# Performance work log

Hardware: AMD Instinct MI355X
Metric: run time of the kernel (lower is better)

## Reference

```python
import jax, jax.numpy as jnp
import numpy as np

T, B = 100, 256
NUM_IN, NUM_HID, NUM_OUT = 784, 512, 10
BETA = 0.95
THRESH = 1.0   # snntorch Leaky default threshold
SLOPE = 25.0   # surrogate.fast_sigmoid default slope

# Heaviside spike with fast_sigmoid surrogate gradient (snntorch semantics)
@jax.custom_vjp
def spike_fn(x):
    return (x > 0).astype(x.dtype)

def _spike_fwd(x):
    return spike_fn(x), x

def _spike_bwd(x, g):
    return (g / (SLOPE * jnp.abs(x) + 1.0) ** 2,)

spike_fn.defvjp(_spike_fwd, _spike_bwd)

def setup_inputs() -> dict:
    key = jax.random.key(0)
    ks = jax.random.split(key, 5)
    x = jax.random.normal(ks[0], (T, B, NUM_IN), dtype=jnp.float32)
    w1 = jax.random.normal(ks[1], (NUM_HID, NUM_IN), dtype=jnp.float32) / np.float32(np.sqrt(NUM_IN))
    b1 = jax.random.normal(ks[2], (NUM_HID,), dtype=jnp.float32) * 0.01
    w2 = jax.random.normal(ks[3], (NUM_OUT, NUM_HID), dtype=jnp.float32) / np.float32(np.sqrt(NUM_HID))
    b2 = jax.random.normal(ks[4], (NUM_OUT,), dtype=jnp.float32) * 0.01
    return {"x": x, "w1": w1, "b1": b1, "w2": w2, "b2": b2}

def _snn_forward(x, w1, b1, w2, b2):
    mem1_0 = jnp.zeros((B, NUM_HID), x.dtype)
    mem2_0 = jnp.zeros((B, NUM_OUT), x.dtype)

    def step(carry, xt):
        mem1, mem2 = carry
        # layer 1: Linear + Leaky (reset-by-subtraction, reset detached as in snntorch)
        cur1 = xt @ w1.T + b1
        reset1 = jax.lax.stop_gradient(spike_fn(mem1 - THRESH))
        mem1 = BETA * mem1 + cur1 - reset1 * THRESH
        spk1 = spike_fn(mem1 - THRESH)
        # layer 2
        cur2 = spk1 @ w2.T + b2
        reset2 = jax.lax.stop_gradient(spike_fn(mem2 - THRESH))
        mem2 = BETA * mem2 + cur2 - reset2 * THRESH
        spk2 = spike_fn(mem2 - THRESH)
        return (mem1, mem2), (cur2, spk2, spk1, mem2, mem1)

    _, ys = jax.lax.scan(step, (mem1_0, mem2_0), x)
    # ys = (cur_list, spk_list, spk_hidden_list, mem_list, mem_hidden_list), stacked over T
    return ys

def reference(x, w1, b1, w2, b2):
    return _snn_forward(x, w1, b1, w2, b2)
```

## Files before the change

kernel.cpp:

```cpp
#include <hip/hip_runtime.h>
#include <stdint.h>

#define T_STEPS 100
#define BATCH   256
#define NIN     784
#define NHID    512
#define NOUT    10


#define BM 128
#define BN 128
#define BK 8
#define PANEL_K 384

__global__ __launch_bounds__(256) void gemm1_dual(
    const float* __restrict__ X, const float* __restrict__ W,
    float* __restrict__ C1, float* __restrict__ C2)
{
    __shared__ float As[2][BK][BM + 4];
    __shared__ float Bs[2][BK][BN + 4];

    const int tid = threadIdx.x;
    const int bm  = blockIdx.x * BM;
    const int bn  = blockIdx.y * BN;
    const int kb  = blockIdx.z ? PANEL_K : 0;
    float* __restrict__ C = blockIdx.z ? C2 : C1;

    const int row  = tid >> 1;
    const int koff = (tid & 1) * 4;

    const int w    = tid >> 6;
    const int lane = tid & 63;
    const int tm   = (w & 1) * 64 + (lane & 7) * 8;
    const int tn   = (w >> 1) * 64 + (lane >> 3) * 8;

    float acc[8][8];
    #pragma unroll
    for (int i = 0; i < 8; ++i)
        #pragma unroll
        for (int j = 0; j < 8; ++j) acc[i][j] = 0.f;

    const float* Xp = X + (size_t)(bm + row) * NIN + kb + koff;
    const float* Wp = W + (size_t)(bn + row) * NIN + kb + koff;

    float4 pa = *(const float4*)(Xp);
    float4 pb = *(const float4*)(Wp);
    As[0][koff+0][row] = pa.x; As[0][koff+1][row] = pa.y;
    As[0][koff+2][row] = pa.z; As[0][koff+3][row] = pa.w;
    Bs[0][koff+0][row] = pb.x; Bs[0][koff+1][row] = pb.y;
    Bs[0][koff+2][row] = pb.z; Bs[0][koff+3][row] = pb.w;

    const int NITER = PANEL_K / BK;
    for (int it = 0; it < NITER; ++it) {
        const int cur = it & 1;
        __syncthreads();

        if (it + 1 < NITER) {
            const int k0 = (it + 1) * BK;
            pa = *(const float4*)(Xp + k0);
            pb = *(const float4*)(Wp + k0);
        }

        #pragma unroll
        for (int kk = 0; kk < BK; ++kk) {
            float4 av0 = *(const float4*)&As[cur][kk][tm];
            float4 av1 = *(const float4*)&As[cur][kk][tm + 4];
            float4 bv0 = *(const float4*)&Bs[cur][kk][tn];
            float4 bv1 = *(const float4*)&Bs[cur][kk][tn + 4];
            float a[8] = {av0.x, av0.y, av0.z, av0.w, av1.x, av1.y, av1.z, av1.w};
            float b[8] = {bv0.x, bv0.y, bv0.z, bv0.w, bv1.x, bv1.y, bv1.z, bv1.w};
            #pragma unroll
            for (int i = 0; i < 8; ++i)
                #pragma unroll
                for (int j = 0; j < 8; ++j)
                    acc[i][j] = fmaf(a[i], b[j], acc[i][j]);
        }

        if (it + 1 < NITER) {
            const int nxt = cur ^ 1;
            As[nxt][koff+0][row] = pa.x; As[nxt][koff+1][row] = pa.y;
            As[nxt][koff+2][row] = pa.z; As[nxt][koff+3][row] = pa.w;
            Bs[nxt][koff+0][row] = pb.x; Bs[nxt][koff+1][row] = pb.y;
            Bs[nxt][koff+2][row] = pb.z; Bs[nxt][koff+3][row] = pb.w;
        }
    }

    #pragma unroll
    for (int i = 0; i < 8; ++i) {
        size_t r = (size_t)(bm + tm + i) * NHID + bn + tn;
        *(float4*)&C[r]     = make_float4(acc[i][0], acc[i][1], acc[i][2], acc[i][3]);
        *(float4*)&C[r + 4] = make_float4(acc[i][4], acc[i][5], acc[i][6], acc[i][7]);
    }
}

__global__ __launch_bounds__(256) void leaky_hidden_fused(
    float* __restrict__ mem_io,
    const float* __restrict__ c2,
    float* __restrict__ spk_out,
    const float* __restrict__ X,
    const float* __restrict__ W1,
    const float* __restrict__ b1)
{
    __shared__ float4 xs4[T_STEPS][4];

    const int tid = threadIdx.x;
    const int idx = blockIdx.x * 256 + tid;
    const size_t STRIDE = (size_t)BATCH * NHID;
    const int h  = idx & (NHID - 1);
    const int bb = idx >> 9;

    {
        const float* xbase = X + (size_t)bb * NIN + 768;
        for (int e = tid; e < T_STEPS * 4; e += 256) {
            const int t = e >> 2, q = e & 3;
            xs4[t][q] = *(const float4*)(xbase + (size_t)t * BATCH * NIN + q * 4);
        }
    }

    const float* wp = W1 + (size_t)h * NIN + 768;
    float4 w0 = *(const float4*)(wp);
    float4 w1v = *(const float4*)(wp + 4);
    float4 w2v = *(const float4*)(wp + 8);
    float4 w3v = *(const float4*)(wp + 12);
    const float wt[16] = {w0.x, w0.y, w0.z, w0.w, w1v.x, w1v.y, w1v.z, w1v.w,
                          w2v.x, w2v.y, w2v.z, w2v.w, w3v.x, w3v.y, w3v.z, w3v.w};
    const float bias = b1[h];

    float buf1[16], buf2[16];
    #pragma unroll
    for (int i = 0; i < 16; ++i) {
        buf1[i] = mem_io[idx + (size_t)i * STRIDE];
        buf2[i] = c2[idx + (size_t)i * STRIDE];
    }

    __syncthreads();

    float a3cur;
    {
        float4 v0 = xs4[0][0], v1 = xs4[0][1], v2 = xs4[0][2], v3 = xs4[0][3];
        float a = 0.f;
        a = fmaf(v0.x, wt[0], a);  a = fmaf(v0.y, wt[1], a);
        a = fmaf(v0.z, wt[2], a);  a = fmaf(v0.w, wt[3], a);
        a = fmaf(v1.x, wt[4], a);  a = fmaf(v1.y, wt[5], a);
        a = fmaf(v1.z, wt[6], a);  a = fmaf(v1.w, wt[7], a);
        a = fmaf(v2.x, wt[8], a);  a = fmaf(v2.y, wt[9], a);
        a = fmaf(v2.z, wt[10], a); a = fmaf(v2.w, wt[11], a);
        a = fmaf(v3.x, wt[12], a); a = fmaf(v3.y, wt[13], a);
        a = fmaf(v3.z, wt[14], a); a = fmaf(v3.w, wt[15], a);
        a3cur = a;
    }

    float mem = 0.f;

    #define LH_BODY(T_, J_)                                                   \
    {                                                                         \
        const int t_ = (T_);                                                  \
        const float p1 = buf1[(J_)];                                          \
        const float p2 = buf2[(J_)];                                          \
        if (t_ + 16 < T_STEPS) {                                              \
            buf1[(J_)] = mem_io[idx + (size_t)(t_ + 16) * STRIDE];            \
            buf2[(J_)] = c2[idx + (size_t)(t_ + 16) * STRIDE];                \
        }                                                                     \
        float a3next = 0.f;                                                   \
        if (t_ + 1 < T_STEPS) {                                               \
            float4 v0 = xs4[t_ + 1][0], v1 = xs4[t_ + 1][1];                  \
            float4 v2 = xs4[t_ + 1][2], v3 = xs4[t_ + 1][3];                  \
            float a = 0.f;                                                    \
            a = fmaf(v0.x, wt[0], a);  a = fmaf(v0.y, wt[1], a);              \
            a = fmaf(v0.z, wt[2], a);  a = fmaf(v0.w, wt[3], a);              \
            a = fmaf(v1.x, wt[4], a);  a = fmaf(v1.y, wt[5], a);              \
            a = fmaf(v1.z, wt[6], a);  a = fmaf(v1.w, wt[7], a);              \
            a = fmaf(v2.x, wt[8], a);  a = fmaf(v2.y, wt[9], a);              \
            a = fmaf(v2.z, wt[10], a); a = fmaf(v2.w, wt[11], a);             \
            a = fmaf(v3.x, wt[12], a); a = fmaf(v3.y, wt[13], a);             \
            a3next = a;                                                       \
            a3next = fmaf(v3.z, wt[14], a3next);                              \
            a3next = fmaf(v3.w, wt[15], a3next);                              \
        }                                                                     \
        const float cur = __fadd_rn(__fadd_rn(__fadd_rn(p1, p2), a3cur), bias); \
        const float rst = (mem > 1.0f) ? 1.0f : 0.0f;                         \
        mem = __fsub_rn(__fadd_rn(__fmul_rn(0.95f, mem), cur), rst);          \
        const size_t off = idx + (size_t)t_ * STRIDE;                         \
        spk_out[off] = (mem > 1.0f) ? 1.0f : 0.0f;                            \
        mem_io[off]  = mem;                                                   \
        a3cur = a3next;                                                       \
    }

    for (int tb = 0; tb < 96; tb += 16) {
        LH_BODY(tb + 0, 0)  LH_BODY(tb + 1, 1)  LH_BODY(tb + 2, 2)  LH_BODY(tb + 3, 3)
        LH_BODY(tb + 4, 4)  LH_BODY(tb + 5, 5)  LH_BODY(tb + 6, 6)  LH_BODY(tb + 7, 7)
        LH_BODY(tb + 8, 8)  LH_BODY(tb + 9, 9)  LH_BODY(tb + 10, 10) LH_BODY(tb + 11, 11)
        LH_BODY(tb + 12, 12) LH_BODY(tb + 13, 13) LH_BODY(tb + 14, 14) LH_BODY(tb + 15, 15)
    }
    LH_BODY(96, 0) LH_BODY(97, 1) LH_BODY(98, 2) LH_BODY(99, 3)

    #undef LH_BODY
}

#define G2_ROWS 32

__global__ __launch_bounds__(320) void gemm2_f64(
    const float* __restrict__ spk1, const float* __restrict__ W2,
    const float* __restrict__ b2, float* __restrict__ cur2)
{
    __shared__ float w2s[NOUT * NHID];
    const int tid = threadIdx.x;
    for (int i = tid; i < NOUT * NHID; i += 320) w2s[i] = W2[i];
    __syncthreads();

    const int r = tid / NOUT;
    const int o = tid % NOUT;
    const size_t m = (size_t)blockIdx.x * G2_ROWS + r;
    const float* rowp = spk1 + m * NHID;
    const float* wp   = w2s + o * NHID;
    double dot = 0.0;
    #pragma unroll 4
    for (int k = 0; k < NHID; k += 4) {
        float4 s  = *(const float4*)(rowp + k);
        float4 wv = *(const float4*)(wp + k);
        dot = fma((double)s.x, (double)wv.x, dot);
        dot = fma((double)s.y, (double)wv.y, dot);
        dot = fma((double)s.z, (double)wv.z, dot);
        dot = fma((double)s.w, (double)wv.w, dot);
    }
    cur2[m * NOUT + o] = (float)(dot + (double)b2[o]);
}

__global__ __launch_bounds__(256) void leaky_out_kernel(
    const float* __restrict__ cur2, float* __restrict__ spk2,
    float* __restrict__ mem2)
{
    const int idx = blockIdx.x * blockDim.x + threadIdx.x;
    if (idx >= BATCH * NOUT) return;
    const int STRIDE = BATCH * NOUT;

    float cur[T_STEPS];
    #pragma unroll
    for (int t = 0; t < T_STEPS; ++t)
        cur[t] = cur2[(size_t)t * STRIDE + idx];

    float mem = 0.f;
    #pragma unroll
    for (int t = 0; t < T_STEPS; ++t) {
        const float rst = (mem > 1.0f) ? 1.0f : 0.0f;
        mem = __fsub_rn(__fadd_rn(__fmul_rn(0.95f, mem), cur[t]), rst);
        const size_t off = (size_t)t * STRIDE + idx;
        spk2[off] = (mem > 1.0f) ? 1.0f : 0.0f;
        mem2[off] = mem;
    }
}

extern "C" void kernel_launch(void* const* d_in, const int* in_sizes, int n_in,
                              void* d_out, int out_size, void* d_ws, size_t ws_size,
                              hipStream_t stream) {
    const float* x  = (const float*)d_in[0];
    const float* w1 = (const float*)d_in[1];
    const float* b1 = (const float*)d_in[2];
    const float* w2 = (const float*)d_in[3];
    const float* b2 = (const float*)d_in[4];

    float* out = (float*)d_out;
    float* cur2_out = out;
    float* spk2_out = out + 256000;
    float* spk1_out = out + 512000;
    float* mem2_out = out + 13619200;
    float* mem1_out = out + 13875200;

    const int M = T_STEPS * BATCH;

    const size_t p2_bytes = (size_t)M * NHID * sizeof(float);
    float* p2buf = (d_ws != nullptr && ws_size >= p2_bytes)
                       ? (float*)d_ws : spk1_out;

    dim3 gp(M / BM, NHID / BN, 2);
    gemm1_dual<<<gp, 256, 0, stream>>>(x, w1, mem1_out, p2buf);

    leaky_hidden_fused<<<(BATCH * NHID) / 256, 256, 0, stream>>>(
        mem1_out, p2buf, spk1_out, x, w1, b1);

    gemm2_f64<<<M / G2_ROWS, 320, 0, stream>>>(spk1_out, w2, b2, cur2_out);

    leaky_out_kernel<<<(BATCH * NOUT + 255) / 256, 256, 0, stream>>>(
        cur2_out, spk2_out, mem2_out);
}
```

Baseline: 482.9 us.

## Split hidden leaky kernel into producer and consumer warps with LDS double buffering

```diff
diff --git a/kernel.cpp b/kernel.cpp
--- a/kernel.cpp
+++ b/kernel.cpp
@@ -93,108 +93,122 @@
     }
 }
 
-__global__ __launch_bounds__(256) void leaky_hidden_fused(
+__global__ __launch_bounds__(512) void leaky_hidden_fused(
     float* __restrict__ mem_io,
-    const float* __restrict__ c2,
-    float* __restrict__ spk_out,
+    const float* c2,
+    float* spk_out,
     const float* __restrict__ X,
     const float* __restrict__ W1,
     const float* __restrict__ b1)
 {
     __shared__ float4 xs4[T_STEPS][4];
-
-    const int tid = threadIdx.x;
-    const int idx = blockIdx.x * 256 + tid;
+    __shared__ float  p1s[2][8][256];
+    __shared__ float  p2s[2][8][256];
+
+    const int tid  = threadIdx.x;
+    const int lane256 = tid & 255;
+    const int base = blockIdx.x * 256;
     const size_t STRIDE = (size_t)BATCH * NHID;
-    const int h  = idx & (NHID - 1);
-    const int bb = idx >> 9;
+    const int bb = base >> 9;
+    const size_t col = (size_t)base + lane256;
 
     {
         const float* xbase = X + (size_t)bb * NIN + 768;
-        for (int e = tid; e < T_STEPS * 4; e += 256) {
+        for (int e = tid; e < T_STEPS * 4; e += 512) {
             const int t = e >> 2, q = e & 3;
             xs4[t][q] = *(const float4*)(xbase + (size_t)t * BATCH * NIN + q * 4);
         }
     }
 
-    const float* wp = W1 + (size_t)h * NIN + 768;
-    float4 w0 = *(const float4*)(wp);
-    float4 w1v = *(const float4*)(wp + 4);
-    float4 w2v = *(const float4*)(wp + 8);
-    float4 w3v = *(const float4*)(wp + 12);
-    const float wt[16] = {w0.x, w0.y, w0.z, w0.w, w1v.x, w1v.y, w1v.z, w1v.w,
-                          w2v.x, w2v.y, w2v.z, w2v.w, w3v.x, w3v.y, w3v.z, w3v.w};
-    const float bias = b1[h];
-
-    float buf1[16], buf2[16];
-    #pragma unroll
-    for (int i = 0; i < 16; ++i) {
-        buf1[i] = mem_io[idx + (size_t)i * STRIDE];
-        buf2[i] = c2[idx + (size_t)i * STRIDE];
+    const bool producer = (tid >= 256);
+
+    float wt[16];
+    float bias = 0.f;
+    float mem  = 0.f;
+
+    if (producer) {
+        float v1[8], v2[8];
+        #pragma unroll
+        for (int j = 0; j < 8; ++j) {
+            v1[j] = mem_io[col + (size_t)j * STRIDE];
+            v2[j] = c2[col + (size_t)j * STRIDE];
+        }
+        #pragma unroll
+        for (int j = 0; j < 8; ++j) {
+            p1s[0][j][lane256] = v1[j];
+            p2s[0][j][lane256] = v2[j];
+        }
+    } else {
+        const int h = (int)(col & (NHID - 1));
+        const float* wp = W1 + (size_t)h * NIN + 768;
+        float4 w0  = *(const float4*)(wp);
+        float4 w1v = *(const float4*)(wp + 4);
+        float4 w2v = *(const float4*)(wp + 8);
+        float4 w3v = *(const float4*)(wp + 12);
+        wt[0]=w0.x;  wt[1]=w0.y;  wt[2]=w0.z;  wt[3]=w0.w;
+        wt[4]=w1v.x; wt[5]=w1v.y; wt[6]=w1v.z; wt[7]=w1v.w;
+        wt[8]=w2v.x; wt[9]=w2v.y; wt[10]=w2v.z; wt[11]=w2v.w;
+        wt[12]=w3v.x; wt[13]=w3v.y; wt[14]=w3v.z; wt[15]=w3v.w;
+        bias = b1[h];
     }
 
     __syncthreads();
 
-    float a3cur;
-    {
-        float4 v0 = xs4[0][0], v1 = xs4[0][1], v2 = xs4[0][2], v3 = xs4[0][3];
-        float a = 0.f;
-        a = fmaf(v0.x, wt[0], a);  a = fmaf(v0.y, wt[1], a);
-        a = fmaf(v0.z, wt[2], a);  a = fmaf(v0.w, wt[3], a);
-        a = fmaf(v1.x, wt[4], a);  a = fmaf(v1.y, wt[5], a);
-        a = fmaf(v1.z, wt[6], a);  a = fmaf(v1.w, wt[7], a);
-        a = fmaf(v2.x, wt[8], a);  a = fmaf(v2.y, wt[9], a);
-        a = fmaf(v2.z, wt[10], a); a = fmaf(v2.w, wt[11], a);
-        a = fmaf(v3.x, wt[12], a); a = fmaf(v3.y, wt[13], a);
-        a = fmaf(v3.z, wt[14], a); a = fmaf(v3.w, wt[15], a);
-        a3cur = a;
-    }
-
-    float mem = 0.f;
-
-    #define LH_BODY(T_, J_)                                                   \
-    {                                                                         \
-        const int t_ = (T_);                                                  \
-        const float p1 = buf1[(J_)];                                          \
-        const float p2 = buf2[(J_)];                                          \
-        if (t_ + 16 < T_STEPS) {                                              \
-            buf1[(J_)] = mem_io[idx + (size_t)(t_ + 16) * STRIDE];            \
-            buf2[(J_)] = c2[idx + (size_t)(t_ + 16) * STRIDE];                \
-        }                                                                     \
-        float a3next = 0.f;                                                   \
-        if (t_ + 1 < T_STEPS) {                                               \
-            float4 v0 = xs4[t_ + 1][0], v1 = xs4[t_ + 1][1];                  \
-            float4 v2 = xs4[t_ + 1][2], v3 = xs4[t_ + 1][3];                  \
-            float a = 0.f;                                                    \
-            a = fmaf(v0.x, wt[0], a);  a = fmaf(v0.y, wt[1], a);              \
-            a = fmaf(v0.z, wt[2], a);  a = fmaf(v0.w, wt[3], a);              \
-            a = fmaf(v1.x, wt[4], a);  a = fmaf(v1.y, wt[5], a);              \
-            a = fmaf(v1.z, wt[6], a);  a = fmaf(v1.w, wt[7], a);              \
-            a = fmaf(v2.x, wt[8], a);  a = fmaf(v2.y, wt[9], a);              \
-            a = fmaf(v2.z, wt[10], a); a = fmaf(v2.w, wt[11], a);             \
-            a = fmaf(v3.x, wt[12], a); a = fmaf(v3.y, wt[13], a);             \
-            a3next = a;                                                       \
-            a3next = fmaf(v3.z, wt[14], a3next);                              \
-            a3next = fmaf(v3.w, wt[15], a3next);                              \
-        }                                                                     \
-        const float cur = __fadd_rn(__fadd_rn(__fadd_rn(p1, p2), a3cur), bias); \
-        const float rst = (mem > 1.0f) ? 1.0f : 0.0f;                         \
-        mem = __fsub_rn(__fadd_rn(__fmul_rn(0.95f, mem), cur), rst);          \
-        const size_t off = idx + (size_t)t_ * STRIDE;                         \
-        spk_out[off] = (mem > 1.0f) ? 1.0f : 0.0f;                            \
-        mem_io[off]  = mem;                                                   \
-        a3cur = a3next;                                                       \
-    }
-
-    for (int tb = 0; tb < 96; tb += 16) {
-        LH_BODY(tb + 0, 0)  LH_BODY(tb + 1, 1)  LH_BODY(tb + 2, 2)  LH_BODY(tb + 3, 3)
-        LH_BODY(tb + 4, 4)  LH_BODY(tb + 5, 5)  LH_BODY(tb + 6, 6)  LH_BODY(tb + 7, 7)
-        LH_BODY(tb + 8, 8)  LH_BODY(tb + 9, 9)  LH_BODY(tb + 10, 10) LH_BODY(tb + 11, 11)
-        LH_BODY(tb + 12, 12) LH_BODY(tb + 13, 13) LH_BODY(tb + 14, 14) LH_BODY(tb + 15, 15)
-    }
-    LH_BODY(96, 0) LH_BODY(97, 1) LH_BODY(98, 2) LH_BODY(99, 3)
-
-    #undef LH_BODY
+    for (int c = 0; c <= 12; ++c) {
+        if (producer) {
+            if (c < 12) {
+                const int t0 = (c + 1) * 8;
+                const int nb = (c + 1 == 12) ? 4 : 8;
+                float v1[8], v2[8];
+                #pragma unroll
+                for (int j = 0; j < 8; ++j) {
+                    if (j < nb) {
+                        v1[j] = mem_io[col + (size_t)(t0 + j) * STRIDE];
+                        v2[j] = c2[col + (size_t)(t0 + j) * STRIDE];
+                    }
+                }
+                const int pb = (c + 1) & 1;
+                #pragma unroll
+                for (int j = 0; j < 8; ++j) {
+                    if (j < nb) {
+                        p1s[pb][j][lane256] = v1[j];
+                        p2s[pb][j][lane256] = v2[j];
+                    }
+                }
+            }
+        } else {
+            const int nt = (c == 12) ? 4 : 8;
+            const int cb = c & 1;
+            #pragma unroll
+            for (int j = 0; j < 8; ++j) {
+                if (j < nt) {
+                    const int t = c * 8 + j;
+                    const float p1 = p1s[cb][j][lane256];
+                    const float p2 = p2s[cb][j][lane256];
+                    float4 v0 = xs4[t][0], v1 = xs4[t][1];
+                    float4 v2 = xs4[t][2], v3 = xs4[t][3];
+                    float a = 0.f;
+                    a = fmaf(v0.x, wt[0], a);  a = fmaf(v0.y, wt[1], a);
+                    a = fmaf(v0.z, wt[2], a);  a = fmaf(v0.w, wt[3], a);
+                    a = fmaf(v1.x, wt[4], a);  a = fmaf(v1.y, wt[5], a);
+                    a = fmaf(v1.z, wt[6], a);  a = fmaf(v1.w, wt[7], a);
+                    a = fmaf(v2.x, wt[8], a);  a = fmaf(v2.y, wt[9], a);
+                    a = fmaf(v2.z, wt[10], a); a = fmaf(v2.w, wt[11], a);
+                    a = fmaf(v3.x, wt[12], a); a = fmaf(v3.y, wt[13], a);
+                    a = fmaf(v3.z, wt[14], a); a = fmaf(v3.w, wt[15], a);
+
+                    const float cur = __fadd_rn(__fadd_rn(__fadd_rn(p1, p2), a), bias);
+                    const float rst = (mem > 1.0f) ? 1.0f : 0.0f;
+                    mem = __fsub_rn(__fadd_rn(__fmul_rn(0.95f, mem), cur), rst);
+
+                    const size_t off = col + (size_t)t * STRIDE;
+                    spk_out[off] = (mem > 1.0f) ? 1.0f : 0.0f;
+                    mem_io[off]  = mem;
+                }
+            }
+        }
+        __syncthreads();
+    }
 }
 
 #define G2_ROWS 32
@@ -275,7 +289,7 @@
     dim3 gp(M / BM, NHID / BN, 2);
     gemm1_dual<<<gp, 256, 0, stream>>>(x, w1, mem1_out, p2buf);
 
-    leaky_hidden_fused<<<(BATCH * NHID) / 256, 256, 0, stream>>>(
+    leaky_hidden_fused<<<(BATCH * NHID) / 256, 512, 0, stream>>>(
         mem1_out, p2buf, spk1_out, x, w1, b1);
 
     gemm2_f64<<<M / G2_ROWS, 320, 0, stream>>>(spk1_out, w2, b2, cur2_out);
```

New measurement: 468.9 us. -2.9%, faster.
